# Performance work log

Measured on AMD Instinct MI355X. Metric: run time of the kernel, lower is better.

The kernel has to match this reference:

```python
import jax, jax.numpy as jnp
import numpy as np

D_MODEL = 256
D_STATE = 64
D_CONV = 4
EXPAND = 2
HEADDIM = 64
D_INNER = EXPAND * D_MODEL            # 512
NHEADS = D_INNER // HEADDIM           # 8
D_XBC = D_INNER + 2 * D_STATE         # 640 (x, B, C; ngroups=1)
D_IN_PROJ = 2 * D_INNER + 2 * D_STATE + NHEADS  # 1160


def setup_inputs() -> dict:
    key = jax.random.key(0)
    ks = jax.random.split(key, 8)
    x = jax.random.normal(ks[0], (64, 5000, 12), jnp.float32)
    W_in = jax.random.normal(ks[1], (D_MODEL, D_IN_PROJ), jnp.float32) * 0.02
    conv_w = jax.random.normal(ks[2], (D_XBC, D_CONV), jnp.float32) * 0.1
    conv_b = jnp.zeros((D_XBC,), jnp.float32)
    A_log = jnp.log(jax.random.uniform(ks[3], (NHEADS,), jnp.float32, 1.0, 16.0))
    dt_bias = jax.random.normal(ks[4], (NHEADS,), jnp.float32) * 0.1
    D = jnp.ones((NHEADS,), jnp.float32)
    norm_w = jnp.ones((D_INNER,), jnp.float32)
    W_out = jax.random.normal(ks[5], (D_INNER, D_MODEL), jnp.float32) * 0.02
    return {"x": x, "W_in": W_in, "conv_w": conv_w, "conv_b": conv_b,
            "A_log": A_log, "dt_bias": dt_bias, "D": D,
            "norm_w": norm_w, "W_out": W_out}


def _mamba2(u, W_in, conv_w, conv_b, A_log, dt_bias, D, norm_w, W_out):
    b, l, _ = u.shape
    zxbcdt = u @ W_in                                   # (b,l,1160)
    z = zxbcdt[..., :D_INNER]                           # (b,l,512)
    xBC = zxbcdt[..., D_INNER:D_INNER + D_XBC]          # (b,l,640)
    dt = zxbcdt[..., D_INNER + D_XBC:]                  # (b,l,8)
    # causal depthwise conv1d (kernel 4) + SiLU
    xp = jnp.pad(xBC, ((0, 0), (D_CONV - 1, 0), (0, 0)))
    xBC = sum(xp[:, k:k + l, :] * conv_w[:, k] for k in range(D_CONV)) + conv_b
    xBC = jax.nn.silu(xBC)
    xs = xBC[..., :D_INNER].reshape(b, l, NHEADS, HEADDIM)
    Bm = xBC[..., D_INNER:D_INNER + D_STATE]            # (b,l,64)
    Cm = xBC[..., D_INNER + D_STATE:]                   # (b,l,64)
    dt = jax.nn.softplus(dt + dt_bias)                  # (b,l,h)
    A = -jnp.exp(A_log)                                 # (h,)

    def step(h, inp):
        x_t, dt_t, B_t, C_t = inp                       # (b,h,p),(b,h),(b,n),(b,n)
        decay = jnp.exp(dt_t * A)                       # (b,h)
        h = h * decay[..., None, None] + (dt_t[..., None] * x_t)[..., None] * B_t[:, None, None, :]
        y = jnp.einsum('bhpn,bn->bhp', h, C_t)
        return h, y

    h0 = jnp.zeros((b, NHEADS, HEADDIM, D_STATE), u.dtype)
    _, ys = jax.lax.scan(step, h0, (xs.transpose(1, 0, 2, 3), dt.transpose(1, 0, 2),
                                    Bm.transpose(1, 0, 2), Cm.transpose(1, 0, 2)))
    y = ys.transpose(1, 0, 2, 3) + D[None, None, :, None] * xs   # D skip, per head
    y = y.reshape(b, l, D_INNER)
    # RMSNormGated: gate then rmsnorm
    y = y * jax.nn.silu(z)
    y = y * jax.lax.rsqrt(jnp.mean(y * y, axis=-1, keepdims=True) + 1e-5) * norm_w
    return y @ W_out                                    # (b,l,256)


def reference(x, W_in, conv_w, conv_b, A_log, dt_bias, D, norm_w, W_out):
    b = x.shape[0]
    u = x.reshape(b, 250, 240)                          # 'b (t p1) f -> b t (p1 f)'
    u = jnp.pad(u, ((0, 0), (0, 0), (0, D_MODEL - 240)))
    y = _mamba2(u, W_in, conv_w, conv_b, A_log, dt_bias, D, norm_w, W_out)
    y = jax.nn.selu(y)                                  # AlphaDropout is identity at eval
    y = y[..., :240]
    return y.reshape(b, 5000, 12)
```

## Files before the change

### kernel.cpp

```cpp
#include <hip/hip_runtime.h>
#include <cstdint>
#include <cstddef>

#define D_MODEL 256
#define D_STATE 64
#define HEADDIM 64
#define D_INNER 512
#define NHEADS 8
#define D_XBC 640
#define NPROJ 1160
#define ZXW 1152
#define BATCH 64
#define SEQ 250
#define ROWS (BATCH * SEQ)
#define KIN 240
#define KPAD 256
#define NPAD 1280
#define TPAD 256

typedef __bf16 bf16x8 __attribute__((ext_vector_type(8)));
typedef float f32x4 __attribute__((ext_vector_type(4)));

typedef __attribute__((address_space(1))) const void gv_t;
typedef __attribute__((address_space(3))) void lv_t;

__device__ __forceinline__ float readlane_f(float v, int lane) {
    return __uint_as_float(__builtin_amdgcn_readlane(__float_as_uint(v), lane));
}
__device__ __forceinline__ float silu_f(float x) { return x * (1.f / (1.f + __expf(-x))); }
__device__ __forceinline__ unsigned short bf16_rne(float f) {
    unsigned int u = __float_as_uint(f);
    u += 0x7fff + ((u >> 16) & 1);
    return (unsigned short)(u >> 16);
}
__device__ __forceinline__ float bf2f(unsigned short u) {
    return __uint_as_float(((unsigned int)u) << 16);
}
__device__ __forceinline__ unsigned int pack2(float a, float b) {
    return (unsigned int)bf16_rne(a) | ((unsigned int)bf16_rne(b) << 16);
}

#define NA (ROWS * KPAD)
#define NB (NPAD * KPAD)
#define NW (D_MODEL * D_INNER)
__global__ __launch_bounds__(256) void cast_all_kernel(const float* __restrict__ x,
                                                       const float* __restrict__ Win,
                                                       const float* __restrict__ Wout,
                                                       unsigned short* __restrict__ a_bf,
                                                       unsigned short* __restrict__ bt_bf,
                                                       unsigned short* __restrict__ wt_bf) {
    int idx = blockIdx.x * 256 + threadIdx.x;
    if (idx < NA) {
        int row = idx >> 8, c = idx & 255;
        float v = (c < KIN) ? x[row * KIN + c] : 0.f;
        a_bf[idx] = bf16_rne(v);
    } else if (idx < NA + NB) {
        int r = idx - NA;
        int n = r >> 8, k = r & 255;
        float v = (n < NPROJ && k < KIN) ? Win[k * NPROJ + n] : 0.f;
        bt_bf[r] = bf16_rne(v);
    } else if (idx < NA + NB + NW) {
        int r = idx - NA - NB;
        int n = r & 255, k = r >> 8;
        wt_bf[n * D_INNER + k] = bf16_rne(Wout[k * D_MODEL + n]);
    }
}

__global__ __launch_bounds__(256) void gemm1_mfma(const unsigned short* __restrict__ A,
                                                  const unsigned short* __restrict__ Bt,
                                                  unsigned short* __restrict__ Czx,
                                                  float* __restrict__ dtraw) {
    __shared__ unsigned short As[128 * 32];
    __shared__ unsigned short Bs[128 * 32];
    const int tid = threadIdx.x;
    const int lane = tid & 63, wave = tid >> 6;
    const int wm = wave >> 1, wn = wave & 1;
    const int q = lane >> 4, l15 = lane & 15;
    const int rowBase = blockIdx.y * 128, colBase = blockIdx.x * 128;
    f32x4 acc[4][4] = {};

    const int sr = tid >> 2;
    const int sc = (tid & 3) * 8;

    const unsigned short* gA = A + (size_t)(rowBase + sr) * KPAD + sc;
    const unsigned short* gB = Bt + (size_t)(colBase + sr) * KPAD + sc;
    unsigned short* lA = &As[sr * 32 + sc];
    unsigned short* lB = &Bs[sr * 32 + sc];

    for (int k0 = 0; k0 < KPAD; k0 += 32) {
        __builtin_amdgcn_global_load_lds((gv_t*)(gA + k0), (lv_t*)lA, 16, 0, 0);
        __builtin_amdgcn_global_load_lds((gv_t*)(gA + 64 * KPAD + k0),
                                         (lv_t*)(lA + 64 * 32), 16, 0, 0);
        __builtin_amdgcn_global_load_lds((gv_t*)(gB + k0), (lv_t*)lB, 16, 0, 0);
        __builtin_amdgcn_global_load_lds((gv_t*)(gB + 64 * KPAD + k0),
                                         (lv_t*)(lB + 64 * 32), 16, 0, 0);
        __syncthreads();

        bf16x8 bfr[4];
#pragma unroll
        for (int nt = 0; nt < 4; nt++)
            bfr[nt] = *(const bf16x8*)&Bs[(wn * 64 + nt * 16 + l15) * 32 + q * 8];
#pragma unroll
        for (int mt = 0; mt < 4; mt++) {
            bf16x8 afr = *(const bf16x8*)&As[(wm * 64 + mt * 16 + l15) * 32 + q * 8];
#pragma unroll
            for (int nt = 0; nt < 4; nt++)
                acc[mt][nt] = __builtin_amdgcn_mfma_f32_16x16x32_bf16(afr, bfr[nt],
                                                                      acc[mt][nt], 0, 0, 0);
        }
        __syncthreads();
    }
#pragma unroll
    for (int mt = 0; mt < 4; mt++) {
        int grow0 = rowBase + wm * 64 + mt * 16 + q * 4;
#pragma unroll
        for (int nt = 0; nt < 4; nt++) {
            int gcol = colBase + wn * 64 + nt * 16 + l15;
            if (gcol < ZXW) {
#pragma unroll
                for (int reg = 0; reg < 4; reg++) {
                    unsigned int u = bf16_rne(acc[mt][nt][reg]);
                    unsigned int partner = (unsigned int)__shfl_xor((int)u, 1, 64);
                    if ((l15 & 1) == 0)
                        *(unsigned int*)&Czx[(size_t)(grow0 + reg) * ZXW + gcol] =
                            u | (partner << 16);
                }
            } else if (gcol < NPROJ) {
#pragma unroll
                for (int reg = 0; reg < 4; reg++)
                    dtraw[(size_t)(grow0 + reg) * NHEADS + (gcol - ZXW)] = acc[mt][nt][reg];
            }
        }
    }
}

#define CT_IN_STR 68
#define CT_TR_STR 70
__global__ __launch_bounds__(256) void conv_kernel(const unsigned short* __restrict__ zxbc,
                                                   const float* __restrict__ dtraw,
                                                   const float* __restrict__ conv_w,
                                                   const float* __restrict__ conv_b,
                                                   const float* __restrict__ dt_bias,
                                                   unsigned short* __restrict__ xc_bf,
                                                   unsigned short* __restrict__ xcT_bf,
                                                   float* __restrict__ dtp) {
    const int b = blockIdx.x;
    const int t0 = blockIdx.z * 64;
    if (blockIdx.y == 10) {
        for (int it = threadIdx.x; it < 512; it += 256) {
            int h = it & 7;
            int t = t0 + (it >> 3);
            if (t < SEQ) {
                float v = dtraw[(size_t)(b * SEQ + t) * NHEADS + h] + dt_bias[h];
                dtp[(size_t)(b * SEQ + t) * NHEADS + h] =
                    (v > 20.f) ? v : __logf(1.f + __expf(v));
            }
        }
        return;
    }
    __shared__ float In[67 * CT_IN_STR];
    __shared__ unsigned short OutT[64 * CT_TR_STR];
    const int cg = blockIdx.y;
    const int tid = threadIdx.x;
    const int lane = tid & 63;
    const int w = tid >> 6;
    const int ch = cg * 64 + lane;

    for (int r = w; r < 67; r += 4) {
        int t = t0 - 3 + r;
        float v = (t >= 0 && t < SEQ)
                      ? bf2f(zxbc[(size_t)(b * SEQ + t) * ZXW + D_INNER + ch])
                      : 0.f;
        In[r * CT_IN_STR + lane] = v;
    }
    __syncthreads();
    const float w0 = conv_w[ch * 4 + 0], w1 = conv_w[ch * 4 + 1];
    const float w2 = conv_w[ch * 4 + 2], w3 = conv_w[ch * 4 + 3];
    const float bias = conv_b[ch];
    unsigned short vals[16];
#pragma unroll
    for (int i = 0; i < 16; i++) {
        int tt = w * 16 + i;
        float acc = fmaf(w3, In[(tt + 3) * CT_IN_STR + lane],
                    fmaf(w2, In[(tt + 2) * CT_IN_STR + lane],
                    fmaf(w1, In[(tt + 1) * CT_IN_STR + lane],
                    fmaf(w0, In[tt * CT_IN_STR + lane], bias))));
        float sv = silu_f(acc);
        unsigned short bv = (t0 + tt < SEQ) ? bf16_rne(sv) : (unsigned short)0;
        vals[i] = bv;
        OutT[lane * CT_TR_STR + tt] = bv;
    }
    if (cg >= 8) {
#pragma unroll
        for (int i = 0; i < 16; i++) {
            int tt = w * 16 + i;
            if (t0 + tt < SEQ)
                xc_bf[(size_t)(b * SEQ + t0 + tt) * D_XBC + ch] = vals[i];
        }
    }
    if (cg <= 8) {
        __syncthreads();
        unsigned short* dstbase = xcT_bf + ((size_t)b * D_XBC + cg * 64) * TPAD + t0;
#pragma unroll
        for (int i = 0; i < 16; i++) {
            int c2 = w * 16 + i;
            dstbase[(size_t)c2 * TPAD + lane] = OutT[c2 * CT_TR_STR + lane];
        }
    }
}

#define LSTR 72
__global__ __launch_bounds__(256) void scan_fused(const unsigned short* __restrict__ xc_bf,
                                                  const unsigned short* __restrict__ xcT_bf,
                                                  const float* __restrict__ dtp,
                                                  const float* __restrict__ A_log,
                                                  const float* __restrict__ Dvec,
                                                  unsigned short* __restrict__ yout_bf) {
    __shared__ unsigned short C_l[64 * LSTR];
    __shared__ unsigned short BP_l[64 * LSTR];
    __shared__ unsigned short XT_l[64 * LSTR];
    __shared__ unsigned short H_l[64 * LSTR];
    __shared__ float cs_s[64], dts_s[64], fws_s[64];
    __shared__ float tot_s;

    const int bh = blockIdx.x;
    const int b = bh >> 3, h = bh & 7;
    const int tid = threadIdx.x;
    const int lane = tid & 63, w = tid >> 6;
    const int q = lane >> 4, l15 = lane & 15;
    const float A = -__expf(A_log[h]);
    const float Dh = Dvec[h];
    const int r = tid >> 2, c0 = (tid & 3) * 16;

    f32x4 h_acc[4] = {};

    for (int c = 0; c < 4; ++c) {
        const int t0 = c * 64;
        if (c > 0) __syncthreads();

        if (t0 + r < SEQ) {
            const unsigned short* rowp = xc_bf + (size_t)(b * SEQ + t0 + r) * D_XBC;
            *(uint4*)&C_l[r * LSTR + c0] = *(const uint4*)&rowp[D_INNER + D_STATE + c0];
            *(uint4*)&C_l[r * LSTR + c0 + 8] =
                *(const uint4*)&rowp[D_INNER + D_STATE + c0 + 8];
            *(uint4*)&BP_l[r * LSTR + c0] = *(const uint4*)&rowp[D_INNER + c0];
            *(uint4*)&BP_l[r * LSTR + c0 + 8] = *(const uint4*)&rowp[D_INNER + c0 + 8];
        } else {
            uint4 z = {0, 0, 0, 0};
            *(uint4*)&C_l[r * LSTR + c0] = z;
            *(uint4*)&C_l[r * LSTR + c0 + 8] = z;
            *(uint4*)&BP_l[r * LSTR + c0] = z;
            *(uint4*)&BP_l[r * LSTR + c0 + 8] = z;
        }
        {
            const unsigned short* xrow =
                xcT_bf + ((size_t)b * D_XBC + h * HEADDIM + r) * TPAD + t0;
            *(uint4*)&XT_l[r * LSTR + c0] = *(const uint4*)&xrow[c0];
            *(uint4*)&XT_l[r * LSTR + c0 + 8] = *(const uint4*)&xrow[c0 + 8];
        }
        uint4 braw0, braw1;
        {
            const unsigned short* brow =
                xcT_bf + ((size_t)b * D_XBC + D_INNER + r) * TPAD + t0 + c0;
            braw0 = *(const uint4*)&brow[0];
            braw1 = *(const uint4*)&brow[8];
        }
        if (w == 0) {
            int t = lane;
            float dtv = (t0 + t < SEQ) ? dtp[(size_t)(b * SEQ + t0 + t) * NHEADS + h] : 0.f;
            float csv = dtv * A;
#pragma unroll
            for (int o = 1; o < 64; o <<= 1) {
                float u = __shfl_up(csv, o, 64);
                if (lane >= o) csv += u;
            }
            float tot = readlane_f(csv, 63);
            cs_s[t] = csv;
            dts_s[t] = dtv;
            fws_s[t] = dtv * __expf(tot - csv);
            if (lane == 0) tot_s = tot;
        }
        __syncthreads();

        f32x4 g[4] = {};
        f32x4 yi[4] = {};
#pragma unroll
        for (int k0 = 0; k0 < 64; k0 += 32) {
            bf16x8 ca = *(const bf16x8*)&C_l[(w * 16 + l15) * LSTR + k0 + q * 8];
#pragma unroll
            for (int nt = 0; nt < 4; nt++) {
                bf16x8 bb = *(const bf16x8*)&BP_l[(nt * 16 + l15) * LSTR + k0 + q * 8];
                g[nt] = __builtin_amdgcn_mfma_f32_16x16x32_bf16(ca, bb, g[nt], 0, 0, 0);
            }
            if (c > 0) {
#pragma unroll
                for (int nt = 0; nt < 4; nt++) {
                    bf16x8 hb = *(const bf16x8*)&H_l[(nt * 16 + l15) * LSTR + k0 + q * 8];
                    yi[nt] = __builtin_amdgcn_mfma_f32_16x16x32_bf16(ca, hb, yi[nt], 0, 0, 0);
                }
            }
        }
        __syncthreads();

        {
            unsigned short tmp[16];
            const unsigned short* rp = (const unsigned short*)&braw0;
#pragma unroll
            for (int j = 0; j < 8; j++) tmp[j] = bf16_rne(bf2f(rp[j]) * fws_s[c0 + j]);
            rp = (const unsigned short*)&braw1;
#pragma unroll
            for (int j = 0; j < 8; j++) tmp[8 + j] = bf16_rne(bf2f(rp[j]) * fws_s[c0 + 8 + j]);
            *(uint4*)&C_l[r * LSTR + c0] = *(uint4*)&tmp[0];
            *(uint4*)&C_l[r * LSTR + c0 + 8] = *(uint4*)&tmp[8];
        }
#pragma unroll
        for (int nt = 0; nt < 4; nt++) {
#pragma unroll
            for (int rr = 0; rr < 4; rr++) {
                int t = w * 16 + q * 4 + rr;
                int s = nt * 16 + l15;
                float pv = 0.f;
                if (s <= t) {
                    pv = g[nt][rr] * __expf(cs_s[t] - cs_s[s]) * dts_s[s];
                    if (s == t) pv += Dh;
                }
                unsigned int u = bf16_rne(pv);
                unsigned int partner = (unsigned int)__shfl_xor((int)u, 1, 64);
                if ((l15 & 1) == 0)
                    *(unsigned int*)&BP_l[t * LSTR + nt * 16 + l15] = u | (partner << 16);
            }
        }
        __syncthreads();

        f32x4 y[4] = {};
#pragma unroll
        for (int k0 = 0; k0 < 64; k0 += 32) {
            bf16x8 pa = *(const bf16x8*)&BP_l[(w * 16 + l15) * LSTR + k0 + q * 8];
#pragma unroll
            for (int nt = 0; nt < 4; nt++) {
                bf16x8 xb = *(const bf16x8*)&XT_l[(nt * 16 + l15) * LSTR + k0 + q * 8];
                y[nt] = __builtin_amdgcn_mfma_f32_16x16x32_bf16(pa, xb, y[nt], 0, 0, 0);
            }
        }
        if (c < 3) {
            f32x4 st[4] = {};
#pragma unroll
            for (int k0 = 0; k0 < 64; k0 += 32) {
                bf16x8 xa = *(const bf16x8*)&XT_l[(w * 16 + l15) * LSTR + k0 + q * 8];
#pragma unroll
                for (int nt = 0; nt < 4; nt++) {
                    bf16x8 bwb = *(const bf16x8*)&C_l[(nt * 16 + l15) * LSTR + k0 + q * 8];
                    st[nt] = __builtin_amdgcn_mfma_f32_16x16x32_bf16(xa, bwb, st[nt], 0, 0, 0);
                }
            }
            const float decay = __expf(tot_s);
#pragma unroll
            for (int nt = 0; nt < 4; nt++) {
                h_acc[nt] = st[nt] + decay * h_acc[nt];
#pragma unroll
                for (int rr = 0; rr < 4; rr++) {
                    unsigned int u = bf16_rne(h_acc[nt][rr]);
                    unsigned int partner = (unsigned int)__shfl_xor((int)u, 1, 64);
                    if ((l15 & 1) == 0)
                        *(unsigned int*)&H_l[(w * 16 + q * 4 + rr) * LSTR + nt * 16 + l15] =
                            u | (partner << 16);
                }
            }
        }
#pragma unroll
        for (int nt = 0; nt < 4; nt++)
#pragma unroll
            for (int rr = 0; rr < 4; rr++) {
                int t = w * 16 + q * 4 + rr;
                if (t0 + t < SEQ) {
                    int p = nt * 16 + l15;
                    float yv = y[nt][rr];
                    if (c > 0) yv += __expf(cs_s[t]) * yi[nt][rr];
                    unsigned int u = bf16_rne(yv);
                    unsigned int partner = (unsigned int)__shfl_xor((int)u, 1, 64);
                    if ((l15 & 1) == 0)
                        *(unsigned int*)&yout_bf[(size_t)(b * SEQ + t0 + t) * D_INNER +
                                                 h * HEADDIM + p] = u | (partner << 16);
                }
            }
    }
}

#define SA 40
__global__ __launch_bounds__(256) void gemm2_fused(const unsigned short* __restrict__ yout_bf,
                                                   const unsigned short* __restrict__ zxbc,
                                                   const unsigned short* __restrict__ Bt,
                                                   const float* __restrict__ norm_w,
                                                   float* __restrict__ out) {
    __shared__ unsigned short As2[32 * SA];
    __shared__ unsigned short Bs2[256 * SA];
    __shared__ float rms_s[32];
    const int tid = threadIdx.x;
    const int lane = tid & 63;
    const int wn = tid >> 6;
    const int q = lane >> 4, l15 = lane & 15;
    const int rowBase = blockIdx.x * 32;
    f32x4 acc[2][4] = {};

    const int tr = tid >> 3;
    const int tk = (tid & 7) * 4;

    const unsigned short* yrow = yout_bf + (size_t)(rowBase + tr) * D_INNER + tk;
    const unsigned short* zrow = zxbc + (size_t)(rowBase + tr) * ZXW + tk;
    float ssq = 0.f;

    for (int k0 = 0; k0 < D_INNER; k0 += 32) {
        uint2 yp = *(const uint2*)&yrow[k0];
        uint2 zp = *(const uint2*)&zrow[k0];
        float4 nw = *(const float4*)&norm_w[k0 + tk];
        const unsigned short* ys = (const unsigned short*)&yp;
        const unsigned short* zs = (const unsigned short*)&zp;
        float g0 = bf2f(ys[0]) * silu_f(bf2f(zs[0]));
        float g1 = bf2f(ys[1]) * silu_f(bf2f(zs[1]));
        float g2 = bf2f(ys[2]) * silu_f(bf2f(zs[2]));
        float g3 = bf2f(ys[3]) * silu_f(bf2f(zs[3]));
        ssq = fmaf(g0, g0, ssq);
        ssq = fmaf(g1, g1, ssq);
        ssq = fmaf(g2, g2, ssq);
        ssq = fmaf(g3, g3, ssq);
        uint2 pk;
        pk.x = pack2(g0 * nw.x, g1 * nw.y);
        pk.y = pack2(g2 * nw.z, g3 * nw.w);
        *(uint2*)&As2[tr * SA + tk] = pk;
        const unsigned short* brow = Bt + (size_t)tid * D_INNER + k0;
        *(uint4*)&Bs2[tid * SA + 0] = *(const uint4*)&brow[0];
        *(uint4*)&Bs2[tid * SA + 8] = *(const uint4*)&brow[8];
        *(uint4*)&Bs2[tid * SA + 16] = *(const uint4*)&brow[16];
        *(uint4*)&Bs2[tid * SA + 24] = *(const uint4*)&brow[24];
        __syncthreads();

        bf16x8 bfr[4];
#pragma unroll
        for (int nt = 0; nt < 4; nt++)
            bfr[nt] = *(const bf16x8*)&Bs2[(wn * 64 + nt * 16 + l15) * SA + q * 8];
#pragma unroll
        for (int mt = 0; mt < 2; mt++) {
            bf16x8 afr = *(const bf16x8*)&As2[(mt * 16 + l15) * SA + q * 8];
#pragma unroll
            for (int nt = 0; nt < 4; nt++)
                acc[mt][nt] = __builtin_amdgcn_mfma_f32_16x16x32_bf16(afr, bfr[nt],
                                                                      acc[mt][nt], 0, 0, 0);
        }
        __syncthreads();
    }
    ssq += __shfl_xor(ssq, 1, 64);
    ssq += __shfl_xor(ssq, 2, 64);
    ssq += __shfl_xor(ssq, 4, 64);
    if ((tid & 7) == 0) rms_s[tr] = rsqrtf(ssq * (1.f / 512.f) + 1e-5f);
    __syncthreads();

    const float SC = 1.0507009873554805f, AL = 1.6732632423543772f;
#pragma unroll
    for (int mt = 0; mt < 2; mt++) {
        int lrow0 = mt * 16 + q * 4;
#pragma unroll
        for (int nt = 0; nt < 4; nt++) {
            int gcol = wn * 64 + nt * 16 + l15;
            if (gcol < 240) {
#pragma unroll
                for (int reg = 0; reg < 4; reg++) {
                    float v = acc[mt][nt][reg] * rms_s[lrow0 + reg];
                    v = (v > 0.f) ? SC * v : SC * AL * (__expf(v) - 1.f);
                    out[(size_t)(rowBase + lrow0 + reg) * 240 + gcol] = v;
                }
            }
        }
    }
}

extern "C" void kernel_launch(void* const* d_in, const int* in_sizes, int n_in,
                              void* d_out, int out_size, void* d_ws, size_t ws_size,
                              hipStream_t stream) {
    const float* x = (const float*)d_in[0];
    const float* W_in = (const float*)d_in[1];
    const float* conv_w = (const float*)d_in[2];
    const float* conv_b = (const float*)d_in[3];
    const float* A_log = (const float*)d_in[4];
    const float* dt_bias = (const float*)d_in[5];
    const float* Dv = (const float*)d_in[6];
    const float* norm_w = (const float*)d_in[7];
    const float* W_out = (const float*)d_in[8];
    float* out = (float*)d_out;

    unsigned short* us = (unsigned short*)d_ws;
    unsigned short* zxbc_bf = us;
    unsigned short* xc_bf = zxbc_bf + (size_t)ROWS * ZXW;
    unsigned short* xcT_bf = xc_bf + (size_t)ROWS * D_XBC;
    unsigned short* yout_bf = xcT_bf + (size_t)BATCH * D_XBC * TPAD;
    unsigned short* st_g = yout_bf + (size_t)ROWS * D_INNER;
    unsigned short* bt_bf = st_g + (size_t)512 * 3 * 4096;
    unsigned short* wt_bf = bt_bf + (size_t)NPAD * KPAD;
    float* dtraw = (float*)(wt_bf + (size_t)D_MODEL * D_INNER);
    float* dtp = dtraw + (size_t)ROWS * NHEADS;
    unsigned short* a_bf = (unsigned short*)(dtp + (size_t)ROWS * NHEADS);

    int cast_total = NA + NB + NW;
    cast_all_kernel<<<dim3((cast_total + 255) / 256), 256, 0, stream>>>(x, W_in, W_out,
                                                                        a_bf, bt_bf, wt_bf);

    gemm1_mfma<<<dim3(NPAD / 128, ROWS / 128), 256, 0, stream>>>(a_bf, bt_bf, zxbc_bf, dtraw);

    conv_kernel<<<dim3(BATCH, 11, 4), 256, 0, stream>>>(zxbc_bf, dtraw, conv_w, conv_b,
                                                        dt_bias, xc_bf, xcT_bf, dtp);

    scan_fused<<<dim3(BATCH * NHEADS), 256, 0, stream>>>(xc_bf, xcT_bf, dtp, A_log, Dv,
                                                         yout_bf);

    gemm2_fused<<<dim3(ROWS / 32), 256, 0, stream>>>(yout_bf, zxbc_bf, wt_bf, norm_w, out);
}
```

Before: 194.5 us.

## Fuse causal conv1d, SiLU and softplus into the chunked scan kernel

```diff
diff --git a/kernel.cpp b/kernel.cpp
--- a/kernel.cpp
+++ b/kernel.cpp
@@ -16,7 +16,6 @@
 #define KIN 240
 #define KPAD 256
 #define NPAD 1280
-#define TPAD 256
 
 typedef __bf16 bf16x8 __attribute__((ext_vector_type(8)));
 typedef float f32x4 __attribute__((ext_vector_type(4)));
@@ -134,85 +133,13 @@
     }
 }
 
-#define CT_IN_STR 68
-#define CT_TR_STR 70
-__global__ __launch_bounds__(256) void conv_kernel(const unsigned short* __restrict__ zxbc,
-                                                   const float* __restrict__ dtraw,
-                                                   const float* __restrict__ conv_w,
-                                                   const float* __restrict__ conv_b,
-                                                   const float* __restrict__ dt_bias,
-                                                   unsigned short* __restrict__ xc_bf,
-                                                   unsigned short* __restrict__ xcT_bf,
-                                                   float* __restrict__ dtp) {
-    const int b = blockIdx.x;
-    const int t0 = blockIdx.z * 64;
-    if (blockIdx.y == 10) {
-        for (int it = threadIdx.x; it < 512; it += 256) {
-            int h = it & 7;
-            int t = t0 + (it >> 3);
-            if (t < SEQ) {
-                float v = dtraw[(size_t)(b * SEQ + t) * NHEADS + h] + dt_bias[h];
-                dtp[(size_t)(b * SEQ + t) * NHEADS + h] =
-                    (v > 20.f) ? v : __logf(1.f + __expf(v));
-            }
-        }
-        return;
-    }
-    __shared__ float In[67 * CT_IN_STR];
-    __shared__ unsigned short OutT[64 * CT_TR_STR];
-    const int cg = blockIdx.y;
-    const int tid = threadIdx.x;
-    const int lane = tid & 63;
-    const int w = tid >> 6;
-    const int ch = cg * 64 + lane;
-
-    for (int r = w; r < 67; r += 4) {
-        int t = t0 - 3 + r;
-        float v = (t >= 0 && t < SEQ)
-                      ? bf2f(zxbc[(size_t)(b * SEQ + t) * ZXW + D_INNER + ch])
-                      : 0.f;
-        In[r * CT_IN_STR + lane] = v;
-    }
-    __syncthreads();
-    const float w0 = conv_w[ch * 4 + 0], w1 = conv_w[ch * 4 + 1];
-    const float w2 = conv_w[ch * 4 + 2], w3 = conv_w[ch * 4 + 3];
-    const float bias = conv_b[ch];
-    unsigned short vals[16];
-#pragma unroll
-    for (int i = 0; i < 16; i++) {
-        int tt = w * 16 + i;
-        float acc = fmaf(w3, In[(tt + 3) * CT_IN_STR + lane],
-                    fmaf(w2, In[(tt + 2) * CT_IN_STR + lane],
-                    fmaf(w1, In[(tt + 1) * CT_IN_STR + lane],
-                    fmaf(w0, In[tt * CT_IN_STR + lane], bias))));
-        float sv = silu_f(acc);
-        unsigned short bv = (t0 + tt < SEQ) ? bf16_rne(sv) : (unsigned short)0;
-        vals[i] = bv;
-        OutT[lane * CT_TR_STR + tt] = bv;
-    }
-    if (cg >= 8) {
-#pragma unroll
-        for (int i = 0; i < 16; i++) {
-            int tt = w * 16 + i;
-            if (t0 + tt < SEQ)
-                xc_bf[(size_t)(b * SEQ + t0 + tt) * D_XBC + ch] = vals[i];
-        }
-    }
-    if (cg <= 8) {
-        __syncthreads();
-        unsigned short* dstbase = xcT_bf + ((size_t)b * D_XBC + cg * 64) * TPAD + t0;
-#pragma unroll
-        for (int i = 0; i < 16; i++) {
-            int c2 = w * 16 + i;
-            dstbase[(size_t)c2 * TPAD + lane] = OutT[c2 * CT_TR_STR + lane];
-        }
-    }
-}
-
 #define LSTR 72
-__global__ __launch_bounds__(256) void scan_fused(const unsigned short* __restrict__ xc_bf,
-                                                  const unsigned short* __restrict__ xcT_bf,
-                                                  const float* __restrict__ dtp,
+#define INSTR 200
+__global__ __launch_bounds__(256) void scan_fused(const unsigned short* __restrict__ zxbc,
+                                                  const float* __restrict__ dtraw,
+                                                  const float* __restrict__ conv_w,
+                                                  const float* __restrict__ conv_b,
+                                                  const float* __restrict__ dt_bias,
                                                   const float* __restrict__ A_log,
                                                   const float* __restrict__ Dvec,
                                                   unsigned short* __restrict__ yout_bf) {
@@ -220,6 +147,9 @@
     __shared__ unsigned short BP_l[64 * LSTR];
     __shared__ unsigned short XT_l[64 * LSTR];
     __shared__ unsigned short H_l[64 * LSTR];
+    __shared__ unsigned short In_l[67 * INSTR];
+    __shared__ float Wk_l[4][INSTR];
+    __shared__ float Bi_l[192];
     __shared__ float cs_s[64], dts_s[64], fws_s[64];
     __shared__ float tot_s;
 
@@ -230,44 +160,37 @@
     const int q = lane >> 4, l15 = lane & 15;
     const float A = -__expf(A_log[h]);
     const float Dh = Dvec[h];
-    const int r = tid >> 2, c0 = (tid & 3) * 16;
+    const float dtb = dt_bias[h];
+
+    for (int i = tid; i < 192; i += 256) {
+        int xbc = (i < 64) ? (h * 64 + i) : (448 + i);
+        Bi_l[i] = conv_b[xbc];
+#pragma unroll
+        for (int k = 0; k < 4; k++) Wk_l[k][i] = conv_w[xbc * 4 + k];
+    }
 
     f32x4 h_acc[4] = {};
 
     for (int c = 0; c < 4; ++c) {
         const int t0 = c * 64;
-        if (c > 0) __syncthreads();
-
-        if (t0 + r < SEQ) {
-            const unsigned short* rowp = xc_bf + (size_t)(b * SEQ + t0 + r) * D_XBC;
-            *(uint4*)&C_l[r * LSTR + c0] = *(const uint4*)&rowp[D_INNER + D_STATE + c0];
-            *(uint4*)&C_l[r * LSTR + c0 + 8] =
-                *(const uint4*)&rowp[D_INNER + D_STATE + c0 + 8];
-            *(uint4*)&BP_l[r * LSTR + c0] = *(const uint4*)&rowp[D_INNER + c0];
-            *(uint4*)&BP_l[r * LSTR + c0 + 8] = *(const uint4*)&rowp[D_INNER + c0 + 8];
-        } else {
-            uint4 z = {0, 0, 0, 0};
-            *(uint4*)&C_l[r * LSTR + c0] = z;
-            *(uint4*)&C_l[r * LSTR + c0 + 8] = z;
-            *(uint4*)&BP_l[r * LSTR + c0] = z;
-            *(uint4*)&BP_l[r * LSTR + c0 + 8] = z;
-        }
-        {
-            const unsigned short* xrow =
-                xcT_bf + ((size_t)b * D_XBC + h * HEADDIM + r) * TPAD + t0;
-            *(uint4*)&XT_l[r * LSTR + c0] = *(const uint4*)&xrow[c0];
-            *(uint4*)&XT_l[r * LSTR + c0 + 8] = *(const uint4*)&xrow[c0 + 8];
-        }
-        uint4 braw0, braw1;
-        {
-            const unsigned short* brow =
-                xcT_bf + ((size_t)b * D_XBC + D_INNER + r) * TPAD + t0 + c0;
-            braw0 = *(const uint4*)&brow[0];
-            braw1 = *(const uint4*)&brow[8];
+        __syncthreads();
+
+        for (int i = tid; i < 67 * 24; i += 256) {
+            int r = i / 24, s = i - r * 24;
+            int tg = t0 - 3 + r;
+            int colg = (s < 8) ? (D_INNER + h * 64 + s * 8) : (D_INNER + 512 + (s - 8) * 8);
+            uint4 v = {0, 0, 0, 0};
+            if (tg >= 0 && tg < SEQ)
+                v = *(const uint4*)&zxbc[(size_t)(b * SEQ + tg) * ZXW + colg];
+            *(uint4*)&In_l[r * INSTR + s * 8] = v;
         }
         if (w == 0) {
             int t = lane;
-            float dtv = (t0 + t < SEQ) ? dtp[(size_t)(b * SEQ + t0 + t) * NHEADS + h] : 0.f;
+            float dtv = 0.f;
+            if (t0 + t < SEQ) {
+                float v = dtraw[(size_t)(b * SEQ + t0 + t) * NHEADS + h] + dtb;
+                dtv = (v > 20.f) ? v : __logf(1.f + __expf(v));
+            }
             float csv = dtv * A;
 #pragma unroll
             for (int o = 1; o < 64; o <<= 1) {
@@ -282,6 +205,61 @@
         }
         __syncthreads();
 
+        const int cA = lane;
+        const int base = w * 16;
+        unsigned int bpk[8];
+        {
+            const float wx0 = Wk_l[0][cA], wx1 = Wk_l[1][cA], wx2 = Wk_l[2][cA],
+                        wx3 = Wk_l[3][cA], bx = Bi_l[cA];
+            const float wb0 = Wk_l[0][64 + cA], wb1 = Wk_l[1][64 + cA],
+                        wb2 = Wk_l[2][64 + cA], wb3 = Wk_l[3][64 + cA], bb = Bi_l[64 + cA];
+            const float wc0 = Wk_l[0][128 + cA], wc1 = Wk_l[1][128 + cA],
+                        wc2 = Wk_l[2][128 + cA], wc3 = Wk_l[3][128 + cA], bc = Bi_l[128 + cA];
+            float x0 = bf2f(In_l[(base + 0) * INSTR + cA]);
+            float x1 = bf2f(In_l[(base + 1) * INSTR + cA]);
+            float x2 = bf2f(In_l[(base + 2) * INSTR + cA]);
+            float b0 = bf2f(In_l[(base + 0) * INSTR + 64 + cA]);
+            float b1 = bf2f(In_l[(base + 1) * INSTR + 64 + cA]);
+            float b2 = bf2f(In_l[(base + 2) * INSTR + 64 + cA]);
+            float c0v = bf2f(In_l[(base + 0) * INSTR + 128 + cA]);
+            float c1v = bf2f(In_l[(base + 1) * INSTR + 128 + cA]);
+            float c2v = bf2f(In_l[(base + 2) * INSTR + 128 + cA]);
+            unsigned int xu[8];
+            unsigned int lox = 0, lob = 0;
+#pragma unroll
+            for (int j = 0; j < 16; j++) {
+                const int t = base + j;
+                const bool valid = (t0 + t < SEQ);
+                float x3 = bf2f(In_l[(t + 3) * INSTR + cA]);
+                float ax = fmaf(wx3, x3, fmaf(wx2, x2, fmaf(wx1, x1, fmaf(wx0, x0, bx))));
+                float sx = valid ? silu_f(ax) : 0.f;
+                x0 = x1; x1 = x2; x2 = x3;
+                float b3 = bf2f(In_l[(t + 3) * INSTR + 64 + cA]);
+                float ab = fmaf(wb3, b3, fmaf(wb2, b2, fmaf(wb1, b1, fmaf(wb0, b0, bb))));
+                float sb = valid ? silu_f(ab) : 0.f;
+                b0 = b1; b1 = b2; b2 = b3;
+                float c3v = bf2f(In_l[(t + 3) * INSTR + 128 + cA]);
+                float ac = fmaf(wc3, c3v, fmaf(wc2, c2v, fmaf(wc1, c1v, fmaf(wc0, c0v, bc))));
+                float sc = valid ? silu_f(ac) : 0.f;
+                c0v = c1v; c1v = c2v; c2v = c3v;
+                unsigned int ux = bf16_rne(sx);
+                if (j & 1) xu[j >> 1] = lox | (ux << 16); else lox = ux;
+                unsigned int ub = bf16_rne(sb);
+                unsigned int pb = (unsigned int)__shfl_xor((int)ub, 1, 64);
+                if (!(cA & 1)) *(unsigned int*)&BP_l[t * LSTR + cA] = ub | (pb << 16);
+                if (j & 1) bpk[j >> 1] = lob | (ub << 16); else lob = ub;
+                unsigned int uc = bf16_rne(sc);
+                unsigned int pc = (unsigned int)__shfl_xor((int)uc, 1, 64);
+                if (!(cA & 1)) *(unsigned int*)&C_l[t * LSTR + cA] = uc | (pc << 16);
+            }
+            uint4 xa0, xa1;
+            xa0.x = xu[0]; xa0.y = xu[1]; xa0.z = xu[2]; xa0.w = xu[3];
+            xa1.x = xu[4]; xa1.y = xu[5]; xa1.z = xu[6]; xa1.w = xu[7];
+            *(uint4*)&XT_l[cA * LSTR + base] = xa0;
+            *(uint4*)&XT_l[cA * LSTR + base + 8] = xa1;
+        }
+        __syncthreads();
+
         f32x4 g[4] = {};
         f32x4 yi[4] = {};
 #pragma unroll
@@ -289,8 +267,8 @@
             bf16x8 ca = *(const bf16x8*)&C_l[(w * 16 + l15) * LSTR + k0 + q * 8];
 #pragma unroll
             for (int nt = 0; nt < 4; nt++) {
-                bf16x8 bb = *(const bf16x8*)&BP_l[(nt * 16 + l15) * LSTR + k0 + q * 8];
-                g[nt] = __builtin_amdgcn_mfma_f32_16x16x32_bf16(ca, bb, g[nt], 0, 0, 0);
+                bf16x8 bb2 = *(const bf16x8*)&BP_l[(nt * 16 + l15) * LSTR + k0 + q * 8];
+                g[nt] = __builtin_amdgcn_mfma_f32_16x16x32_bf16(ca, bb2, g[nt], 0, 0, 0);
             }
             if (c > 0) {
 #pragma unroll
@@ -304,14 +282,14 @@
 
         {
             unsigned short tmp[16];
-            const unsigned short* rp = (const unsigned short*)&braw0;
-#pragma unroll
-            for (int j = 0; j < 8; j++) tmp[j] = bf16_rne(bf2f(rp[j]) * fws_s[c0 + j]);
-            rp = (const unsigned short*)&braw1;
-#pragma unroll
-            for (int j = 0; j < 8; j++) tmp[8 + j] = bf16_rne(bf2f(rp[j]) * fws_s[c0 + 8 + j]);
-            *(uint4*)&C_l[r * LSTR + c0] = *(uint4*)&tmp[0];
-            *(uint4*)&C_l[r * LSTR + c0 + 8] = *(uint4*)&tmp[8];
+#pragma unroll
+            for (int j = 0; j < 8; j++) {
+                unsigned int v = bpk[j];
+                tmp[2 * j] = bf16_rne(bf2f((unsigned short)(v & 0xffff)) * fws_s[base + 2 * j]);
+                tmp[2 * j + 1] = bf16_rne(bf2f((unsigned short)(v >> 16)) * fws_s[base + 2 * j + 1]);
+            }
+            *(uint4*)&C_l[cA * LSTR + base] = *(uint4*)&tmp[0];
+            *(uint4*)&C_l[cA * LSTR + base + 8] = *(uint4*)&tmp[8];
         }
 #pragma unroll
         for (int nt = 0; nt < 4; nt++) {
@@ -489,15 +467,11 @@
 
     unsigned short* us = (unsigned short*)d_ws;
     unsigned short* zxbc_bf = us;
-    unsigned short* xc_bf = zxbc_bf + (size_t)ROWS * ZXW;
-    unsigned short* xcT_bf = xc_bf + (size_t)ROWS * D_XBC;
-    unsigned short* yout_bf = xcT_bf + (size_t)BATCH * D_XBC * TPAD;
-    unsigned short* st_g = yout_bf + (size_t)ROWS * D_INNER;
-    unsigned short* bt_bf = st_g + (size_t)512 * 3 * 4096;
+    unsigned short* yout_bf = zxbc_bf + (size_t)ROWS * ZXW;
+    unsigned short* bt_bf = yout_bf + (size_t)ROWS * D_INNER;
     unsigned short* wt_bf = bt_bf + (size_t)NPAD * KPAD;
     float* dtraw = (float*)(wt_bf + (size_t)D_MODEL * D_INNER);
-    float* dtp = dtraw + (size_t)ROWS * NHEADS;
-    unsigned short* a_bf = (unsigned short*)(dtp + (size_t)ROWS * NHEADS);
+    unsigned short* a_bf = (unsigned short*)(dtraw + (size_t)ROWS * NHEADS);
 
     int cast_total = NA + NB + NW;
     cast_all_kernel<<<dim3((cast_total + 255) / 256), 256, 0, stream>>>(x, W_in, W_out,
@@ -505,11 +479,8 @@
 
     gemm1_mfma<<<dim3(NPAD / 128, ROWS / 128), 256, 0, stream>>>(a_bf, bt_bf, zxbc_bf, dtraw);
 
-    conv_kernel<<<dim3(BATCH, 11, 4), 256, 0, stream>>>(zxbc_bf, dtraw, conv_w, conv_b,
-                                                        dt_bias, xc_bf, xcT_bf, dtp);
-
-    scan_fused<<<dim3(BATCH * NHEADS), 256, 0, stream>>>(xc_bf, xcT_bf, dtp, A_log, Dv,
-                                                         yout_bf);
+    scan_fused<<<dim3(BATCH * NHEADS), 256, 0, stream>>>(zxbc_bf, dtraw, conv_w, conv_b,
+                                                         dt_bias, A_log, Dv, yout_bf);
 
     gemm2_fused<<<dim3(ROWS / 32), 256, 0, stream>>>(yout_bf, zxbc_bf, wt_bf, norm_w, out);
 }
```

Result: slower. 201.1 us (+3.4%).
